# Kernel tuning notes

Measured on AMD Instinct MI355X. Metric: run time of the kernel, lower is better.

The kernel has to match this reference:

```python
import jax, jax.numpy as jnp
import numpy as np

B, S, H, G, W_LOC = 2, 4096, 12, 64, 513  # Longformer-base: window=2*256+1, 64 global slots


def setup_inputs() -> dict:
    key = jax.random.key(0)
    k1, = jax.random.split(key, 1)
    attention_probs = jax.random.uniform(k1, (B, S, H, G + W_LOC), dtype=jnp.float32)
    attention_mask = jnp.zeros((B, S), dtype=jnp.float32)  # all tokens currently kept
    # global tokens are the first G positions of every batch; nonzero(as_tuple) index arrays
    b_idx = jnp.repeat(jnp.arange(B, dtype=jnp.int64), G)
    g_idx = jnp.tile(jnp.arange(G, dtype=jnp.int64), B)
    return {
        "attention_mask": attention_mask,
        "attention_probs": attention_probs,
        "keep_threshold": jnp.asarray(0.005, dtype=jnp.float32),  # base 0.01*6/12 + learned 0
        "max_num_global_attn_indices": G,
        "loc_b": b_idx, "loc_i": g_idx,
        "glob_b": b_idx, "glob_i": g_idx,
    }


def reference(attention_mask, attention_probs, keep_threshold,
              max_num_global_attn_indices, loc_b, loc_i, glob_b, glob_i):
    Gn = max_num_global_attn_indices
    b, s, h, wg = attention_probs.shape
    w = wg - Gn  # local window size, odd
    half = w // 2

    # zero out rows of already-masked tokens (attention_mask < 0)
    probs = jnp.where((attention_mask < 0)[:, :, None, None], 0.0, attention_probs)

    gl = probs[..., :Gn]                              # [B,S,H,G]
    lo = jnp.transpose(probs[..., Gn:], (0, 2, 1, 3))  # [B,H,S,W]

    # anti-diagonal (key-column) sums of the local band; equals the source's
    # conv2d-with-flipped-identity + slice: out[j] = sum_c lo[j + half - c, c]
    lo_p = jnp.pad(lo, ((0, 0), (0, 0), (half, half), (0, 0)))  # [B,H,S+W-1,W]
    rows = jnp.arange(s)[:, None] + (w - 1) - jnp.arange(w)[None, :]  # [S,W]
    diag = lo_p[:, :, rows, jnp.arange(w)[None, :]]  # [B,H,S,W]
    local_sum = diag.sum(axis=(1, 3))                # [B,S] (summed over heads too)

    global_sum = gl.sum(axis=(1, 2))                 # [B,G]
    probs_sum = local_sum.at[loc_b, loc_i].add(global_sum[glob_b, glob_i])

    probs_max = probs_sum.max(axis=-1, keepdims=True)
    scores = probs_sum / probs_max

    thr = jnp.maximum(jnp.float32(1e-5), jnp.asarray(keep_threshold, jnp.float32).reshape(()))
    new_attention_mask = jnp.where(scores < thr, jnp.float32(-10000.0), jnp.float32(0.0))
    return new_attention_mask, scores
```

## Files before the change

kernel.cpp:

```cpp
#include <hip/hip_runtime.h>
#include <float.h>

#define Bsz 2
#define Ssz 4096
#define Hsz 12
#define Gsz 64
#define Wsz 513
#define Csz (Gsz + Wsz)
#define ROW (Hsz * Csz)
#define HALF 256
#define RPB 8
#define WIN (RPB + Wsz - 1)

#define PSUM_SZ ((size_t)Bsz * Ssz)
#define GACC_SZ ((size_t)Bsz * Gsz)

__global__ __launch_bounds__(256) void k1_fused(
    const float* __restrict__ probs, const float* __restrict__ mask,
    float* __restrict__ psum, float* __restrict__ gacc)
{
    __shared__ float win[WIN];
    const int t = threadIdx.x;
    const int row0 = blockIdx.x * RPB;
    const int b = row0 / Ssz;
    float g = 0.f;
    const bool c2ok = (t < Csz - 512);

    for (int w = t; w < WIN; w += 256) win[w] = 0.f;
    __syncthreads();

    for (int r = 0; r < RPB; ++r) {
        const int row = row0 + r;
        const float* __restrict__ base = probs + (size_t)row * ROW;
        const float scale = (mask[row] < 0.f) ? 0.f : 1.f;

        float a[Hsz], bb[Hsz], c[Hsz];
        #pragma unroll
        for (int h = 0; h < Hsz; ++h) {
            const float* __restrict__ hp = base + h * Csz;
            a[h]  = hp[t];
            bb[h] = hp[t + 256];
            c[h]  = c2ok ? hp[t + 512] : 0.f;
        }

        float v0 = 0.f, v1 = 0.f, v2 = 0.f;
        #pragma unroll
        for (int h = 0; h < Hsz; ++h) { v0 += a[h]; v1 += bb[h]; v2 += c[h]; }
        v0 *= scale; v1 *= scale; v2 *= scale;

        if (t < Gsz) g += v0;
        else atomicAdd(&win[(t - Gsz) + r], v0);
        atomicAdd(&win[(t + 256 - Gsz) + r], v1);
        if (c2ok)
            atomicAdd(&win[(t + 512 - Gsz) + r], v2);
    }
    __syncthreads();

    const int i_base = (row0 - b * Ssz) - HALF;
    for (int w = t; w < WIN; w += 256) {
        const int i = i_base + w;
        if (i >= 0 && i < Ssz) atomicAdd(&psum[b * Ssz + i], win[w]);
    }
    if (t < Gsz) atomicAdd(&gacc[b * Gsz + t], g);
}

__global__ __launch_bounds__(1024) void k4_final(
    const float* __restrict__ psum, const float* __restrict__ thr_p,
    const int* __restrict__ loc_b, const int* __restrict__ loc_i,
    const int* __restrict__ glob_b, const int* __restrict__ glob_i,
    const float* __restrict__ gacc, int n_idx,
    float* __restrict__ out)
{
    const int b = blockIdx.x;
    const int t = threadIdx.x;
    __shared__ float sp[Ssz];
    const float* p = psum + (size_t)b * Ssz;

    for (int i = t; i < Ssz; i += 1024) sp[i] = p[i];
    __syncthreads();

    for (int k = t; k < n_idx; k += 1024)
        if (loc_b[k] == b)
            atomicAdd(&sp[loc_i[k]], gacc[glob_b[k] * Gsz + glob_i[k]]);
    __syncthreads();

    float m = -FLT_MAX;
    for (int i = t; i < Ssz; i += 1024) m = fmaxf(m, sp[i]);
    #pragma unroll
    for (int off = 32; off >= 1; off >>= 1) m = fmaxf(m, __shfl_down(m, off, 64));

    __shared__ float red[16];
    const int wave = t >> 6, lane = t & 63;
    if (lane == 0) red[wave] = m;
    __syncthreads();
    if (t == 0) {
        float mm = red[0];
        #pragma unroll
        for (int w = 1; w < 16; ++w) mm = fmaxf(mm, red[w]);
        red[0] = mm;
    }
    __syncthreads();
    const float mx = red[0];
    const float thr = fmaxf(1e-5f, thr_p[0]);

    for (int i = t; i < Ssz; i += 1024) {
        float sc = sp[i] / mx;
        out[(size_t)Bsz * Ssz + (size_t)b * Ssz + i] = sc;
        out[(size_t)b * Ssz + i] = (sc < thr) ? -10000.f : 0.f;
    }
}

extern "C" void kernel_launch(void* const* d_in, const int* in_sizes, int n_in,
                              void* d_out, int out_size, void* d_ws, size_t ws_size,
                              hipStream_t stream)
{
    const float* mask  = (const float*)d_in[0];
    const float* probs = (const float*)d_in[1];
    const float* thr   = (const float*)d_in[2];
    const int* loc_b  = (const int*)d_in[4];
    const int* loc_i  = (const int*)d_in[5];
    const int* glob_b = (const int*)d_in[6];
    const int* glob_i = (const int*)d_in[7];
    const int n_idx = in_sizes[4];

    float* psum = (float*)d_ws;
    float* gacc = psum + PSUM_SZ;
    float* out  = (float*)d_out;

    hipMemsetAsync(psum, 0, (PSUM_SZ + GACC_SZ) * sizeof(float), stream);

    k1_fused<<<dim3(Bsz * Ssz / RPB), dim3(256), 0, stream>>>(probs, mask, psum, gacc);
    k4_final<<<dim3(Bsz), dim3(1024), 0, stream>>>(psum, thr, loc_b, loc_i,
                                                   glob_b, glob_i, gacc, n_idx, out);
}
```

Measured before the change: 334.3 us.

## Double-buffer row loads into LDS via async global_load_lds pipeline

Replaces direct per-thread global loads of each row with asynchronous global-to-LDS copies into two shared buffers, prefetching the next row while summing the current one. Explicit vmcnt waits and barriers coordinate the stages. The aim is to hide HBM latency in a bandwidth-bound reduction. In exchange it uses about 55KB of LDS per block, which reduces occupancy, and adds extra barriers.

```diff
diff --git a/kernel.cpp b/kernel.cpp
--- a/kernel.cpp
+++ b/kernel.cpp
@@ -8,51 +8,98 @@
 #define Wsz 513
 #define Csz (Gsz + Wsz)
 #define ROW (Hsz * Csz)
+#define ROWB (ROW * 4)
 #define HALF 256
 #define RPB 8
 #define WIN (RPB + Wsz - 1)
 
+#define NCHUNK 27
+#define TAILOFF (NCHUNK * 1024)
+
 #define PSUM_SZ ((size_t)Bsz * Ssz)
 #define GACC_SZ ((size_t)Bsz * Gsz)
+
+typedef const __attribute__((address_space(1))) void* gptr_t;
+typedef __attribute__((address_space(3))) void* lptr_t;
+
+__device__ __forceinline__ void stage_row(const char* rowbase, float* buf,
+                                          int wave, int lane)
+{
+    char* lb = (char*)buf;
+    #pragma unroll
+    for (int j = 0; j < 7; ++j) {
+        const int k = wave + 4 * j;
+        if (k < NCHUNK)
+            __builtin_amdgcn_global_load_lds(
+                (gptr_t)(rowbase + k * 1024 + lane * 16),
+                (lptr_t)(lb + k * 1024), 16, 0, 0);
+    }
+    if (wave == 3 && lane < 3)
+        __builtin_amdgcn_global_load_lds(
+            (gptr_t)(rowbase + TAILOFF + lane * 16),
+            (lptr_t)(lb + TAILOFF), 16, 0, 0);
+}
 
 __global__ __launch_bounds__(256) void k1_fused(
     const float* __restrict__ probs, const float* __restrict__ mask,
     float* __restrict__ psum, float* __restrict__ gacc)
 {
+    __shared__ __align__(16) float bufA[ROW];
+    __shared__ __align__(16) float bufB[ROW];
     __shared__ float win[WIN];
     const int t = threadIdx.x;
+    const int wave = t >> 6, lane = t & 63;
     const int row0 = blockIdx.x * RPB;
     const int b = row0 / Ssz;
     float g = 0.f;
     const bool c2ok = (t < Csz - 512);
 
     for (int w = t; w < WIN; w += 256) win[w] = 0.f;
+
+    float sc[RPB];
+    #pragma unroll
+    for (int r = 0; r < RPB; ++r) {
+        sc[r] = (mask[row0 + r] < 0.f) ? 0.f : 1.f;
+        asm volatile("" :: "v"(sc[r]));
+    }
     __syncthreads();
 
+    const char* pb = (const char*)probs;
+    stage_row(pb + (size_t)row0 * ROWB, bufA, wave, lane);
+
+    #pragma unroll
     for (int r = 0; r < RPB; ++r) {
-        const int row = row0 + r;
-        const float* __restrict__ base = probs + (size_t)row * ROW;
-        const float scale = (mask[row] < 0.f) ? 0.f : 1.f;
+        float* cur = (r & 1) ? bufB : bufA;
+        float* nxt = (r & 1) ? bufA : bufB;
 
-        float a[Hsz], bb[Hsz], c[Hsz];
-        #pragma unroll
-        for (int h = 0; h < Hsz; ++h) {
-            const float* __restrict__ hp = base + h * Csz;
-            a[h]  = hp[t];
-            bb[h] = hp[t + 256];
-            c[h]  = c2ok ? hp[t + 512] : 0.f;
+        if (r + 1 < RPB) {
+            stage_row(pb + (size_t)(row0 + r + 1) * ROWB, nxt, wave, lane);
+            asm volatile("s_waitcnt vmcnt(7)" ::: "memory");
+        } else {
+            asm volatile("s_waitcnt vmcnt(0)" ::: "memory");
         }
+        __builtin_amdgcn_sched_barrier(0);
+        __builtin_amdgcn_s_barrier();
 
         float v0 = 0.f, v1 = 0.f, v2 = 0.f;
         #pragma unroll
-        for (int h = 0; h < Hsz; ++h) { v0 += a[h]; v1 += bb[h]; v2 += c[h]; }
-        v0 *= scale; v1 *= scale; v2 *= scale;
+        for (int h = 0; h < Hsz; ++h) {
+            v0 += cur[h * Csz + t];
+            v1 += cur[h * Csz + t + 256];
+        }
+        if (c2ok) {
+            #pragma unroll
+            for (int h = 0; h < Hsz; ++h) v2 += cur[h * Csz + t + 512];
+        }
+        v0 *= sc[r]; v1 *= sc[r]; v2 *= sc[r];
 
         if (t < Gsz) g += v0;
         else atomicAdd(&win[(t - Gsz) + r], v0);
         atomicAdd(&win[(t + 256 - Gsz) + r], v1);
         if (c2ok)
             atomicAdd(&win[(t + 512 - Gsz) + r], v2);
+
+        __builtin_amdgcn_s_barrier();
     }
     __syncthreads();
 
@@ -127,7 +174,7 @@
     float* gacc = psum + PSUM_SZ;
     float* out  = (float*)d_out;
 
-    hipMemsetAsync(psum, 0, (PSUM_SZ + GACC_SZ) * sizeof(float), stream);
+    (void)hipMemsetAsync(psum, 0, (PSUM_SZ + GACC_SZ) * sizeof(float), stream);
 
     k1_fused<<<dim3(Bsz * Ssz / RPB), dim3(256), 0, stream>>>(probs, mask, psum, gacc);
     k4_final<<<dim3(Bsz), dim3(1024), 0, stream>>>(psum, thr, loc_b, loc_i,
```

After: 331.4 us, median of 2. No clear change (-0.9%).

## Split head reduction into separate streaming kernel before diagonal accumulation

Applied to the files above, without the earlier changes.

Adds a grid-stride kernel that sums the 12 heads for every (row, column) into a row-sum buffer in workspace. The diagonal/window accumulation kernel then reads only these per-row sums, and each block now handles 16 rows instead of 8. The goal is to decouple the bulk, bandwidth-heavy read of the probabilities from the shared-memory atomic stage, so the big read gets more independent loads in flight. In exchange it adds an extra write and read of a roughly 19 MB intermediate buffer. The fixed iteration count also covers slightly more elements than exist, so the last threads read and write past the end of the buffers.

```diff
diff --git a/kernel.cpp b/kernel.cpp
--- a/kernel.cpp
+++ b/kernel.cpp
@@ -9,44 +9,61 @@
 #define Csz (Gsz + Wsz)
 #define ROW (Hsz * Csz)
 #define HALF 256
-#define RPB 8
-#define WIN (RPB + Wsz - 1)
 
 #define PSUM_SZ ((size_t)Bsz * Ssz)
 #define GACC_SZ ((size_t)Bsz * Gsz)
+#define ROWSUM_SZ ((size_t)Bsz * Ssz * Csz)
 
-__global__ __launch_bounds__(256) void k1_fused(
-    const float* __restrict__ probs, const float* __restrict__ mask,
+#define K1A_BLOCKS 2052
+#define K1A_STRIDE (K1A_BLOCKS * 256u)
+#define K1A_ITERS 9
+
+__global__ __launch_bounds__(256) void k1a_hsum(
+    const float* __restrict__ probs, float* __restrict__ rowsum)
+{
+    const unsigned o0 = blockIdx.x * 256u + threadIdx.x;
+    #pragma unroll 2
+    for (int it = 0; it < K1A_ITERS; ++it) {
+        const unsigned o = o0 + (unsigned)it * K1A_STRIDE;
+        const unsigned row = o / Csz;
+        const unsigned c = o - row * Csz;
+        const float* __restrict__ p = probs + (size_t)row * ROW + c;
+
+        float a[Hsz];
+        #pragma unroll
+        for (int h = 0; h < Hsz; ++h) a[h] = p[h * Csz];
+        float v = 0.f;
+        #pragma unroll
+        for (int h = 0; h < Hsz; ++h) v += a[h];
+        rowsum[o] = v;
+    }
+}
+
+#define RPB2 16
+#define WIN2 (RPB2 + Wsz - 1)
+__global__ __launch_bounds__(256) void k1b_diag(
+    const float* __restrict__ rowsum, const float* __restrict__ mask,
     float* __restrict__ psum, float* __restrict__ gacc)
 {
-    __shared__ float win[WIN];
+    __shared__ float win[WIN2];
     const int t = threadIdx.x;
-    const int row0 = blockIdx.x * RPB;
+    const int row0 = blockIdx.x * RPB2;
     const int b = row0 / Ssz;
     float g = 0.f;
     const bool c2ok = (t < Csz - 512);
 
-    for (int w = t; w < WIN; w += 256) win[w] = 0.f;
+    for (int w = t; w < WIN2; w += 256) win[w] = 0.f;
     __syncthreads();
 
-    for (int r = 0; r < RPB; ++r) {
+    #pragma unroll 4
+    for (int r = 0; r < RPB2; ++r) {
         const int row = row0 + r;
-        const float* __restrict__ base = probs + (size_t)row * ROW;
+        const float* __restrict__ base = rowsum + (size_t)row * Csz;
         const float scale = (mask[row] < 0.f) ? 0.f : 1.f;
 
-        float a[Hsz], bb[Hsz], c[Hsz];
-        #pragma unroll
-        for (int h = 0; h < Hsz; ++h) {
-            const float* __restrict__ hp = base + h * Csz;
-            a[h]  = hp[t];
-            bb[h] = hp[t + 256];
-            c[h]  = c2ok ? hp[t + 512] : 0.f;
-        }
-
-        float v0 = 0.f, v1 = 0.f, v2 = 0.f;
-        #pragma unroll
-        for (int h = 0; h < Hsz; ++h) { v0 += a[h]; v1 += bb[h]; v2 += c[h]; }
-        v0 *= scale; v1 *= scale; v2 *= scale;
+        const float v0 = base[t] * scale;
+        const float v1 = base[t + 256] * scale;
+        const float v2 = c2ok ? base[t + 512] * scale : 0.f;
 
         if (t < Gsz) g += v0;
         else atomicAdd(&win[(t - Gsz) + r], v0);
@@ -57,7 +74,7 @@
     __syncthreads();
 
     const int i_base = (row0 - b * Ssz) - HALF;
-    for (int w = t; w < WIN; w += 256) {
+    for (int w = t; w < WIN2; w += 256) {
         const int i = i_base + w;
         if (i >= 0 && i < Ssz) atomicAdd(&psum[b * Ssz + i], win[w]);
     }
@@ -123,13 +140,15 @@
     const int* glob_i = (const int*)d_in[7];
     const int n_idx = in_sizes[4];
 
-    float* psum = (float*)d_ws;
-    float* gacc = psum + PSUM_SZ;
-    float* out  = (float*)d_out;
+    float* psum   = (float*)d_ws;
+    float* gacc   = psum + PSUM_SZ;
+    float* rowsum = gacc + GACC_SZ;
+    float* out    = (float*)d_out;
 
-    hipMemsetAsync(psum, 0, (PSUM_SZ + GACC_SZ) * sizeof(float), stream);
+    (void)hipMemsetAsync(psum, 0, (PSUM_SZ + GACC_SZ) * sizeof(float), stream);
 
-    k1_fused<<<dim3(Bsz * Ssz / RPB), dim3(256), 0, stream>>>(probs, mask, psum, gacc);
+    k1a_hsum<<<dim3(K1A_BLOCKS), dim3(256), 0, stream>>>(probs, rowsum);
+    k1b_diag<<<dim3(Bsz * Ssz / RPB2), dim3(256), 0, stream>>>(rowsum, mask, psum, gacc);
     k4_final<<<dim3(Bsz), dim3(1024), 0, stream>>>(psum, thr, loc_b, loc_i,
                                                    glob_b, glob_i, gacc, n_idx, out);
 }
```

New measurement: 361.2 us. +8.0%, slower.
